# Optimization experiments

Hardware: AMD Instinct MI355X
Metric: run time of the kernel (lower is better)

The kernel has to match this reference:

```python
import math
import jax, jax.numpy as jnp
import numpy as np

B, H, SQ, SK, D, M = 2, 16, 2048, 2048, 128, 128

def setup_inputs() -> dict:
    key = jax.random.key(0)
    kq, kk, ks = jax.random.split(key, 3)
    q = jax.random.normal(kq, (B, H, SQ, D), dtype=jnp.float32)
    k = jax.random.normal(kk, (B, H, SK, D), dtype=jnp.float32)
    # Gaussian projection matrix S of shape (m, dim), as in generate_projection_matrix
    S = jax.random.normal(ks, (M, D), dtype=jnp.float32)
    return {"q": q, "k": k, "S": S}


def reference(q, k, S):
    """QJL: quantize keys to sign bits + norm, then asymmetric inner-product estimate.

    quantize(k):  sign_bits = sign(k @ S.T) with sign(0) -> +1;  norm_k = ||k||_2
    estimate:     <q,k> ~= <S q, sign(S k)> * (sqrt(pi/2)/m) * ||k||
    """
    m = S.shape[0]
    scale = np.float32(math.sqrt(math.pi / 2.0)) / np.float32(m)
    # --- quantize keys ---
    norm_k = jnp.linalg.norm(k, axis=-1)                      # (B,H,SK)
    proj_k = jnp.einsum('bhkd,md->bhkm', k, S)                # (B,H,SK,M)
    sign_bits = jnp.where(proj_k >= 0, 1.0, -1.0).astype(jnp.float32)
    # --- project queries (asymmetric, no quantization) ---
    Sq = jnp.einsum('bhqd,md->bhqm', q, S)                    # (B,H,SQ,M)
    # --- estimate inner products: (Sq * signs).sum(-1) for every (q, k) pair ---
    dots = jnp.einsum('bhqm,bhkm->bhqk', Sq, sign_bits)       # (B,H,SQ,SK)
    estimated = dots * scale * norm_k[:, :, None, :]
    return estimated
```

## Files before the change

### kernel.cpp

```cpp
#include <hip/hip_runtime.h>
#include <hip/hip_bf16.h>
#include <math.h>

#define NBH   32
#define SEQ   2048
#define DD    128
#define MM    128

typedef unsigned short u16;
typedef unsigned int   u32;
typedef float  f32x4  __attribute__((ext_vector_type(4)));
typedef __bf16 bf16x8 __attribute__((ext_vector_type(8)));

#define SCALE_F 0.009791516697777346f
#define TAU 0.18f
#define LCAP 4096

static __device__ __forceinline__ u16 f2bf(float f) {
  union { float f; u32 u; } v; v.f = f;
  u32 u = v.u;
  u += 0x7fffu + ((u >> 16) & 1u);
  return (u16)(u >> 16);
}

static __device__ __forceinline__ void mfma_tile(const u16* lA, const u16* lB,
                                                 int wave, int lane,
                                                 f32x4 acc[4][4]) {
  const int wr = wave >> 1, wc = wave & 1;
  const int lrow = lane & 15, lkg = lane >> 4;
#pragma unroll
  for (int kk = 0; kk < 4; ++kk) {
    bf16x8 af[4], bfr[4];
    const int c = kk * 4 + lkg;
#pragma unroll
    for (int a = 0; a < 4; ++a) {
      const int r  = wr * 64 + a * 16 + lrow;
      const int r2 = wc * 64 + a * 16 + lrow;
      af[a]  = *(const bf16x8*)((const char*)lA + r  * 256 + ((c ^ (r  & 7)) << 4));
      bfr[a] = *(const bf16x8*)((const char*)lB + r2 * 256 + ((c ^ (r2 & 7)) << 4));
    }
#pragma unroll
    for (int a = 0; a < 4; ++a)
#pragma unroll
      for (int b = 0; b < 4; ++b)
        acc[a][b] = __builtin_amdgcn_mfma_f32_16x16x32_bf16(af[a], bfr[b], acc[a][b], 0, 0, 0);
  }
}

static __device__ __forceinline__ void stage_f32_to_bf16(const float* __restrict__ src,
                                                         u16* lds, int tid) {
#pragma unroll
  for (int j = 0; j < 8; ++j) {
    int i = tid + j * 256;
    int r = i >> 4, c = i & 15;
    const f32x4* gp = (const f32x4*)(src + (size_t)r * DD + c * 8);
    f32x4 v0 = gp[0], v1 = gp[1];
    union { u16 h[8]; f32x4 v; } pk;
    pk.h[0] = f2bf(v0.x); pk.h[1] = f2bf(v0.y); pk.h[2] = f2bf(v0.z); pk.h[3] = f2bf(v0.w);
    pk.h[4] = f2bf(v1.x); pk.h[5] = f2bf(v1.y); pk.h[6] = f2bf(v1.z); pk.h[7] = f2bf(v1.w);
    *(f32x4*)((char*)lds + r * 256 + ((c ^ (r & 7)) << 4)) = pk.v;
  }
}

__global__ __launch_bounds__(256) void k_proj(
    const float* __restrict__ Q, const float* __restrict__ K,
    const float* __restrict__ S, u16* __restrict__ Sqb, u16* __restrict__ Sgn,
    float* __restrict__ sn,
    u32* __restrict__ wl, u32* __restrict__ wlcnt, u32 wlcap) {
  __shared__ __align__(16) u16 lA[128 * 128];
  __shared__ __align__(16) u16 lB[128 * 128];
  __shared__ u32 lcnt, lbase;
  const int tid = threadIdx.x;
  const int tile = blockIdx.x;
  const bool isK = (tile >= 512);
  const int row0 = (isK ? (tile - 512) : tile) * 128;
  const float* src = isK ? K : Q;

  if (tid == 0) lcnt = 0;

  stage_f32_to_bf16(S, lB, tid);
  stage_f32_to_bf16(src + (size_t)row0 * DD, lA, tid);

  if (isK) {
    const int row = tid >> 1, half = tid & 1;
    const f32x4* base = (const f32x4*)(src + (size_t)(row0 + row) * DD) + half * 16;
    float s = 0.f;
#pragma unroll
    for (int j = 0; j < 16; ++j) {
      f32x4 v = base[j];
      s += v.x * v.x + v.y * v.y + v.z * v.z + v.w * v.w;
    }
    s += __shfl_xor(s, 1);
    if (half == 0) sn[row0 + row] = SCALE_F * sqrtf(s);
  }
  __syncthreads();

  const int wave = tid >> 6, lane = tid & 63;
  f32x4 acc[4][4];
#pragma unroll
  for (int a = 0; a < 4; ++a)
#pragma unroll
    for (int b = 0; b < 4; ++b) acc[a][b] = (f32x4){0.f, 0.f, 0.f, 0.f};

  mfma_tile(lA, lB, wave, lane, acc);

  __syncthreads();
  u32* lbuf = (u32*)lA;

  const int wr = wave >> 1, wc = wave & 1;
#pragma unroll
  for (int a = 0; a < 4; ++a) {
#pragma unroll
    for (int b = 0; b < 4; ++b) {
      const int rloc = wr * 64 + a * 16 + (lane >> 4) * 4;
      const int m = wc * 64 + b * 16 + (lane & 15);
#pragma unroll
      for (int j = 0; j < 4; ++j) {
        const float v = acc[a][b][j];
        const int row = row0 + rloc + j;
        if (!isK) {
          Sqb[(size_t)row * MM + m] = f2bf(v);
        } else {
          Sgn[(size_t)row * MM + m] = (v >= 0.f) ? 0x3F80 : 0xBF80;
          if (fabsf(v) < TAU && wlcap) {
            u32 p = atomicAdd(&lcnt, 1u);
            u32 code = ((u32)row << 7) | (u32)m;
            if (p < LCAP) lbuf[p] = code;
            else {
              u32 idx = atomicAdd(wlcnt, 1u);
              if (idx < wlcap) wl[idx] = code;
            }
          }
        }
      }
    }
  }

  if (isK && wlcap) {
    __syncthreads();
    if (tid == 0) {
      u32 n = lcnt; if (n > LCAP) n = LCAP;
      lbase = n ? atomicAdd(wlcnt, n) : 0u;
    }
    __syncthreads();
    u32 n = lcnt; if (n > LCAP) n = LCAP;
    for (u32 i = tid; i < n; i += 256) {
      u32 dst = lbase + i;
      if (dst < wlcap) wl[dst] = lbuf[i];
    }
  }
}

__global__ __launch_bounds__(256) void k_fix(
    const float* __restrict__ K, const float* __restrict__ S,
    const u32* __restrict__ wl, const u32* __restrict__ wlcnt,
    u16* __restrict__ Sgn, u32 wlcap) {
  u32 n = *wlcnt; if (n > wlcap) n = wlcap;
  u32 g = blockIdx.x * 256 + threadIdx.x;
  for (u32 e = g; e < n; e += 256u * 1024u) {
    u32 code = wl[e];
    u32 row = code >> 7, m = code & 127u;
    const f32x4* kr = (const f32x4*)(K + (size_t)row * DD);
    const f32x4* sr = (const f32x4*)(S + (size_t)m * DD);
    double acc = 0.0;
#pragma unroll 8
    for (int d = 0; d < 32; ++d) {
      f32x4 a = kr[d], b = sr[d];
      acc += (double)a.x * b.x + (double)a.y * b.y
           + (double)a.z * b.z + (double)a.w * b.w;
    }
    Sgn[(size_t)row * MM + m] = (acc >= 0.0) ? 0x3F80 : 0xBF80;
  }
}

__global__ __launch_bounds__(256) void k_gemm(
    const u16* __restrict__ Sqb, const u16* __restrict__ Sgn,
    const float* __restrict__ sn, float* __restrict__ out) {
  __shared__ __align__(16) u16 lds2[2 * 128 * 128];
  u16* lA = lds2;
  u16* lB = lds2 + 128 * 128;
  const int tid = threadIdx.x;
  const u32 id = blockIdx.x;
  const u32 l = (id & 7) * 1024 + (id >> 3);
  const int tn = l & 15, tm = (l >> 4) & 15, bh = l >> 8;
  const u16* Abase = Sqb + ((size_t)bh * SEQ + tm * 128) * MM;
  const u16* Bbase = Sgn + ((size_t)bh * SEQ + tn * 128) * MM;

  {
    typedef __attribute__((address_space(3))) char lds_t;
    typedef const __attribute__((address_space(1))) char glob_t;
    const int wv = tid >> 6, ln = tid & 63;
#pragma unroll
    for (int j = 0; j < 8; ++j) {
      const int s = j * 256 + wv * 64 + ln;
      const int r = s >> 4, cp = s & 15;
      const int srcoff = r * 256 + ((cp ^ (r & 7)) << 4);
      __builtin_amdgcn_global_load_lds((glob_t*)((const char*)Abase + srcoff),
                                       (lds_t*)((char*)lA + s * 16), 16, 0, 0);
      __builtin_amdgcn_global_load_lds((glob_t*)((const char*)Bbase + srcoff),
                                       (lds_t*)((char*)lB + s * 16), 16, 0, 0);
    }
  }
  __syncthreads();

  const int wave = tid >> 6, lane = tid & 63;
  f32x4 acc[4][4];
#pragma unroll
  for (int a = 0; a < 4; ++a)
#pragma unroll
    for (int b = 0; b < 4; ++b) acc[a][b] = (f32x4){0.f, 0.f, 0.f, 0.f};

  mfma_tile(lA, lB, wave, lane, acc);

  __syncthreads();
  float* lc = (float*)lds2;
  const int wr = wave >> 1, wc = wave & 1;
#pragma unroll
  for (int a = 0; a < 4; ++a) {
#pragma unroll
    for (int b = 0; b < 4; ++b) {
      const int col = wc * 64 + b * 16 + (lane & 15);
#pragma unroll
      for (int j = 0; j < 4; ++j) {
        const int row = wr * 64 + a * 16 + (lane >> 4) * 4 + j;
        lc[row * 128 + (col ^ (((row >> 2) & 1) << 4))] = acc[a][b][j];
      }
    }
  }
  __syncthreads();

  const float* snb = sn + bh * SEQ + tn * 128;
  const size_t outbase = (size_t)bh * SEQ * SEQ + (size_t)tm * 128 * SEQ + tn * 128;
  const int c = tid & 31;
  const int r0 = tid >> 5;
  const f32x4 s4 = *(const f32x4*)(snb + c * 4);
#pragma unroll
  for (int p = 0; p < 16; ++p) {
    const int row = r0 + p * 8;
    const int cs = c ^ (((row >> 2) & 1) << 2);
    f32x4 v = *(const f32x4*)&lc[row * 128 + cs * 4];
    v = v * s4;
    __builtin_nontemporal_store(v, (f32x4*)(out + outbase + (size_t)row * SEQ + c * 4));
  }
}

extern "C" void kernel_launch(void* const* d_in, const int* in_sizes, int n_in,
                              void* d_out, int out_size, void* d_ws, size_t ws_size,
                              hipStream_t stream) {
  const float* q = (const float*)d_in[0];
  const float* k = (const float*)d_in[1];
  const float* S = (const float*)d_in[2];
  float* out = (float*)d_out;
  char* ws = (char*)d_ws;

  const size_t off_Sq  = 0;
  const size_t off_Sg  = 16777216;
  const size_t off_sn  = 33554432;
  const size_t off_cnt = 33849344;
  const size_t off_wl  = 33849600;

  u16*   Sqb = (u16*)(ws + off_Sq);
  u16*   Sgn = (u16*)(ws + off_Sg);
  float* sn  = (float*)(ws + off_sn);
  u32*   cnt = (u32*)(ws + off_cnt);
  u32*   wl  = (u32*)(ws + off_wl);

  u32 wlcap = 0;
  if (ws_size > off_wl + 16) {
    size_t rem = (ws_size - off_wl) / 4;
    wlcap = (u32)(rem > 2097152 ? 2097152 : rem);
  }

  hipMemsetAsync(cnt, 0, 4, stream);
  k_proj<<<1024, 256, 0, stream>>>(q, k, S, Sqb, Sgn, sn, wl, cnt, wlcap);
  k_fix<<<1024, 256, 0, stream>>>(k, S, wl, cnt, Sgn, wlcap);
  k_gemm<<<8192, 256, 0, stream>>>(Sqb, Sgn, sn, out);
}
```

Baseline: 158.0 us.

## Fuse fp64 sign fix-up into projection kernel and vectorize epilogue stores

The separate k_fix kernel, its global worklist, and the memset are removed. Near-zero projections are now queued in a per-block LDS buffer and recomputed in fp64 at the end of k_proj, with an inline fp64 fallback when the buffer overflows. The epilogue also stages the accumulator through swizzled LDS so each thread writes 16-byte rows of Sqb and Sgn instead of scattered 2-byte stores. This saves two launches and the global atomics, at the cost of more LDS per block, possible load imbalance across K blocks, and slow inline fp64 work when a block overflows.

```diff
diff --git a/kernel.cpp b/kernel.cpp
--- a/kernel.cpp
+++ b/kernel.cpp
@@ -14,13 +14,33 @@
 
 #define SCALE_F 0.009791516697777346f
 #define TAU 0.18f
-#define LCAP 4096
+#define CCAP 2048
 
 static __device__ __forceinline__ u16 f2bf(float f) {
   union { float f; u32 u; } v; v.f = f;
   u32 u = v.u;
   u += 0x7fffu + ((u >> 16) & 1u);
   return (u16)(u >> 16);
+}
+
+static __device__ __forceinline__ u16 f64_sign(const float* __restrict__ K,
+                                               const float* __restrict__ S,
+                                               int row_g, int m) {
+  const f32x4* kr = (const f32x4*)(K + (size_t)row_g * DD);
+  const f32x4* sr = (const f32x4*)(S + (size_t)m * DD);
+  double a0 = 0, a1 = 0, a2 = 0, a3 = 0;
+#pragma unroll
+  for (int d = 0; d < 32; d += 4) {
+    f32x4 x0 = kr[d],   y0 = sr[d];
+    f32x4 x1 = kr[d+1], y1 = sr[d+1];
+    f32x4 x2 = kr[d+2], y2 = sr[d+2];
+    f32x4 x3 = kr[d+3], y3 = sr[d+3];
+    a0 += (double)x0.x*y0.x + (double)x0.y*y0.y + (double)x0.z*y0.z + (double)x0.w*y0.w;
+    a1 += (double)x1.x*y1.x + (double)x1.y*y1.y + (double)x1.z*y1.z + (double)x1.w*y1.w;
+    a2 += (double)x2.x*y2.x + (double)x2.y*y2.y + (double)x2.z*y2.z + (double)x2.w*y2.w;
+    a3 += (double)x3.x*y3.x + (double)x3.y*y3.y + (double)x3.z*y3.z + (double)x3.w*y3.w;
+  }
+  return (((a0 + a1) + (a2 + a3)) >= 0.0) ? 0x3F80 : 0xBF80;
 }
 
 static __device__ __forceinline__ void mfma_tile(const u16* lA, const u16* lB,
@@ -65,11 +85,12 @@
 __global__ __launch_bounds__(256) void k_proj(
     const float* __restrict__ Q, const float* __restrict__ K,
     const float* __restrict__ S, u16* __restrict__ Sqb, u16* __restrict__ Sgn,
-    float* __restrict__ sn,
-    u32* __restrict__ wl, u32* __restrict__ wlcnt, u32 wlcap) {
-  __shared__ __align__(16) u16 lA[128 * 128];
-  __shared__ __align__(16) u16 lB[128 * 128];
-  __shared__ u32 lcnt, lbase;
+    float* __restrict__ sn) {
+  __shared__ __align__(16) u16 lds2[2 * 128 * 128];
+  __shared__ u16 cbuf[CCAP];
+  __shared__ u32 lcnt;
+  u16* lA = lds2;
+  u16* lB = lds2 + 128 * 128;
   const int tid = threadIdx.x;
   const int tile = blockIdx.x;
   const bool isK = (tile >= 512);
@@ -105,71 +126,62 @@
   mfma_tile(lA, lB, wave, lane, acc);
 
   __syncthreads();
-  u32* lbuf = (u32*)lA;
-
+  float* lc = (float*)lds2;
   const int wr = wave >> 1, wc = wave & 1;
 #pragma unroll
   for (int a = 0; a < 4; ++a) {
 #pragma unroll
     for (int b = 0; b < 4; ++b) {
-      const int rloc = wr * 64 + a * 16 + (lane >> 4) * 4;
-      const int m = wc * 64 + b * 16 + (lane & 15);
+      const int col = wc * 64 + b * 16 + (lane & 15);
 #pragma unroll
       for (int j = 0; j < 4; ++j) {
-        const float v = acc[a][b][j];
-        const int row = row0 + rloc + j;
-        if (!isK) {
-          Sqb[(size_t)row * MM + m] = f2bf(v);
-        } else {
-          Sgn[(size_t)row * MM + m] = (v >= 0.f) ? 0x3F80 : 0xBF80;
-          if (fabsf(v) < TAU && wlcap) {
-            u32 p = atomicAdd(&lcnt, 1u);
-            u32 code = ((u32)row << 7) | (u32)m;
-            if (p < LCAP) lbuf[p] = code;
-            else {
-              u32 idx = atomicAdd(wlcnt, 1u);
-              if (idx < wlcap) wl[idx] = code;
-            }
-          }
+        const int row = wr * 64 + a * 16 + (lane >> 4) * 4 + j;
+        lc[row * 128 + (col ^ (((row >> 2) & 1) << 4))] = acc[a][b][j];
+      }
+    }
+  }
+  __syncthreads();
+
+  const int c8 = tid & 15;
+  const int rr = tid >> 4;
+#pragma unroll
+  for (int p = 0; p < 8; ++p) {
+    const int row = rr + p * 16;
+    const int s = (row >> 2) & 1;
+    const int cb = (c8 ^ (s << 1)) * 8;
+    f32x4 v0 = *(const f32x4*)&lc[row * 128 + cb];
+    f32x4 v1 = *(const f32x4*)&lc[row * 128 + cb + 4];
+    float vals[8] = {v0.x, v0.y, v0.z, v0.w, v1.x, v1.y, v1.z, v1.w};
+    union { u16 h[8]; f32x4 v; } pk;
+    const int row_g = row0 + row;
+    if (!isK) {
+#pragma unroll
+      for (int e = 0; e < 8; ++e) pk.h[e] = f2bf(vals[e]);
+      *(f32x4*)(Sqb + (size_t)row_g * MM + c8 * 8) = pk.v;
+    } else {
+#pragma unroll
+      for (int e = 0; e < 8; ++e) {
+        const int m = c8 * 8 + e;
+        u16 sg = (vals[e] >= 0.f) ? 0x3F80 : 0xBF80;
+        if (fabsf(vals[e]) < TAU) {
+          u32 pos = atomicAdd(&lcnt, 1u);
+          if (pos < CCAP) cbuf[pos] = (u16)((row << 7) | m);
+          else sg = f64_sign(K, S, row_g, m);
         }
+        pk.h[e] = sg;
       }
-    }
-  }
-
-  if (isK && wlcap) {
+      *(f32x4*)(Sgn + (size_t)row_g * MM + c8 * 8) = pk.v;
+    }
+  }
+
+  if (isK) {
     __syncthreads();
-    if (tid == 0) {
-      u32 n = lcnt; if (n > LCAP) n = LCAP;
-      lbase = n ? atomicAdd(wlcnt, n) : 0u;
-    }
-    __syncthreads();
-    u32 n = lcnt; if (n > LCAP) n = LCAP;
+    u32 n = lcnt; if (n > CCAP) n = CCAP;
     for (u32 i = tid; i < n; i += 256) {
-      u32 dst = lbase + i;
-      if (dst < wlcap) wl[dst] = lbuf[i];
-    }
-  }
-}
-
-__global__ __launch_bounds__(256) void k_fix(
-    const float* __restrict__ K, const float* __restrict__ S,
-    const u32* __restrict__ wl, const u32* __restrict__ wlcnt,
-    u16* __restrict__ Sgn, u32 wlcap) {
-  u32 n = *wlcnt; if (n > wlcap) n = wlcap;
-  u32 g = blockIdx.x * 256 + threadIdx.x;
-  for (u32 e = g; e < n; e += 256u * 1024u) {
-    u32 code = wl[e];
-    u32 row = code >> 7, m = code & 127u;
-    const f32x4* kr = (const f32x4*)(K + (size_t)row * DD);
-    const f32x4* sr = (const f32x4*)(S + (size_t)m * DD);
-    double acc = 0.0;
-#pragma unroll 8
-    for (int d = 0; d < 32; ++d) {
-      f32x4 a = kr[d], b = sr[d];
-      acc += (double)a.x * b.x + (double)a.y * b.y
-           + (double)a.z * b.z + (double)a.w * b.w;
-    }
-    Sgn[(size_t)row * MM + m] = (acc >= 0.0) ? 0x3F80 : 0xBF80;
+      u32 code = cbuf[i];
+      int r = code >> 7, m = code & 127;
+      Sgn[(size_t)(row0 + r) * MM + m] = f64_sign(K, S, row0 + r, m);
+    }
   }
 }
 
@@ -256,23 +268,11 @@
   const size_t off_Sq  = 0;
   const size_t off_Sg  = 16777216;
   const size_t off_sn  = 33554432;
-  const size_t off_cnt = 33849344;
-  const size_t off_wl  = 33849600;
 
   u16*   Sqb = (u16*)(ws + off_Sq);
   u16*   Sgn = (u16*)(ws + off_Sg);
   float* sn  = (float*)(ws + off_sn);
-  u32*   cnt = (u32*)(ws + off_cnt);
-  u32*   wl  = (u32*)(ws + off_wl);
-
-  u32 wlcap = 0;
-  if (ws_size > off_wl + 16) {
-    size_t rem = (ws_size - off_wl) / 4;
-    wlcap = (u32)(rem > 2097152 ? 2097152 : rem);
-  }
-
-  hipMemsetAsync(cnt, 0, 4, stream);
-  k_proj<<<1024, 256, 0, stream>>>(q, k, S, Sqb, Sgn, sn, wl, cnt, wlcap);
-  k_fix<<<1024, 256, 0, stream>>>(k, S, wl, cnt, Sgn, wlcap);
+
+  k_proj<<<1024, 256, 0, stream>>>(q, k, S, Sqb, Sgn, sn);
   k_gemm<<<8192, 256, 0, stream>>>(Sqb, Sgn, sn, out);
 }
```

New measurement: 157.7 us. About the same (-0.2%).
